# Optimization experiments

Measured on AMD Instinct MI355X. Metric: run time of the kernel, lower is better.

Reference implementation:

```python
import jax, jax.numpy as jnp
import numpy as np

H = 16
D_MODEL = 1024
D_HEAD = D_MODEL // H  # 64


def _xavier(key, shape):
    # xavier_uniform over last two dims (matches torch init on [h, in, out])
    fan_in, fan_out = shape[-2], shape[-1]
    limit = float(np.sqrt(6.0 / (fan_in + fan_out)))
    return jax.random.uniform(key, shape, jnp.float32, -limit, limit)


def setup_inputs() -> dict:
    key = jax.random.key(0)
    ks = jax.random.split(key, 7)
    B, S = 4, 2048
    x_q = jax.random.normal(ks[0], (B, S, D_MODEL), jnp.float32)
    x_k = jax.random.normal(ks[1], (B, S, D_MODEL), jnp.float32)
    x_v = jax.random.normal(ks[2], (B, S, D_MODEL), jnp.float32)
    W_Q = _xavier(ks[3], (H, D_MODEL, D_HEAD))
    W_K = _xavier(ks[4], (H, D_MODEL, D_HEAD))
    W_V = _xavier(ks[5], (H, D_MODEL, D_HEAD))
    # torch Linear weight: [out_features, in_features], y = x @ W^T
    lim = float(np.sqrt(6.0 / (2 * D_MODEL)))  # kaiming-uniform-ish default approximated by xavier for reproducibility
    W_O = jax.random.uniform(ks[6], (D_MODEL, D_MODEL), jnp.float32, -lim, lim)
    return {"x_q": x_q, "x_k": x_k, "x_v": x_v,
            "W_Q": W_Q, "W_K": W_K, "W_V": W_V, "W_O": W_O}


def reference(x_q, x_k, x_v, W_Q, W_K, W_V, W_O):
    d_scale = jnp.asarray(D_HEAD, jnp.float32) ** 0.25  # d_q == d_k == dim_q**(1/4)
    # per-head projections: [b,s,m] x [h,m,d] -> [b,h,s,d]
    Q = jnp.einsum('bsm,hmd->bhsd', x_q, W_Q)
    K = jnp.einsum('bsm,hmd->bhsd', x_k, W_K)
    V = jnp.einsum('bsm,hmd->bhsd', x_v, W_V)
    # column softmax over K^T: shape [b,h,d,s], softmax over dim=-2 (the d axis)
    Kt = jnp.swapaxes(K, -1, -2) / d_scale          # [b,h,d,s]
    Kt = jax.nn.softmax(Kt, axis=-2)
    A = jnp.einsum('bhds,bhse->bhde', Kt, V)        # KV precompute [b,h,d,d]
    Qs = jax.nn.softmax(Q / d_scale, axis=-1)       # row softmax over head dim
    Bt = jnp.einsum('bhsd,bhde->bhse', Qs, A)       # [b,h,s,d]
    b, h, s, d = Bt.shape
    # faithful to torch .view on contiguous [b,h,s,d] -> [b,s,h*d] (pure reshape, no transpose)
    Bt = Bt.reshape(b, s, h * d)
    return jnp.einsum('bsi,oi->bso', Bt, W_O)
```

## Files before the change

### kernel.cpp

```cpp
#include <hip/hip_runtime.h>
#include <cstdint>
#include <cstddef>

#define DMODEL 1024
#define HEADS  16
#define DHEAD  64
#define BATCH  4
#define SEQ    2048
#define ROWS   (BATCH * SEQ)
#define INV_DSCALE 0.3535533905932738f

typedef float  f32x4  __attribute__((ext_vector_type(4)));
typedef __bf16 bf16x8 __attribute__((ext_vector_type(8)));
typedef unsigned short u16x8 __attribute__((ext_vector_type(8)));

__device__ __forceinline__ unsigned short f2bf(float x) {
    union { float f; unsigned u; } c; c.f = x;
    unsigned u = c.u;
    return (unsigned short)((u + 0x7fffu + ((u >> 16) & 1u)) >> 16);
}
__device__ __forceinline__ float bf2f(unsigned short h) {
    union { unsigned u; float f; } c; c.u = ((unsigned)h) << 16;
    return c.f;
}

__device__ __forceinline__ void load_g2l16(const unsigned short* g, unsigned short* l) {
    __builtin_amdgcn_global_load_lds(
        (const __attribute__((address_space(1))) unsigned int*)g,
        (__attribute__((address_space(3))) unsigned int*)l,
        16 , 0 , 0 );
}

__global__ __launch_bounds__(256) void cast_bf16(const float4* __restrict__ X,
                                                 ushort4* __restrict__ Y, int n4) {
    int i = blockIdx.x * 256 + threadIdx.x;
    if (i < n4) {
        float4 v = X[i];
        ushort4 o;
        o.x = f2bf(v.x); o.y = f2bf(v.y); o.z = f2bf(v.z); o.w = f2bf(v.w);
        Y[i] = o;
    }
}

__global__ __launch_bounds__(256) void cast3(const float4* __restrict__ x0,
                                             const float4* __restrict__ x1,
                                             const float4* __restrict__ x2,
                                             ushort4* __restrict__ y0,
                                             ushort4* __restrict__ y1,
                                             ushort4* __restrict__ y2) {
    int which = blockIdx.x >> 13;
    int i = ((blockIdx.x & 8191) << 8) + threadIdx.x;
    const float4* X = which == 0 ? x0 : (which == 1 ? x1 : x2);
    ushort4*      Y = which == 0 ? y0 : (which == 1 ? y1 : y2);
    float4 v = X[i];
    ushort4 o;
    o.x = f2bf(v.x); o.y = f2bf(v.y); o.z = f2bf(v.z); o.w = f2bf(v.w);
    Y[i] = o;
}

__global__ __launch_bounds__(256) void pack3(const float* __restrict__ W0,
                                             const float* __restrict__ W1,
                                             const float* __restrict__ W2,
                                             unsigned short* __restrict__ T0,
                                             unsigned short* __restrict__ T1,
                                             unsigned short* __restrict__ T2) {
    __shared__ float tile[64][68];
    int blk = blockIdx.x;
    int w = blk >> 8, h = (blk >> 4) & 15, mb = blk & 15;
    const float* W = w == 0 ? W0 : (w == 1 ? W1 : W2);
    unsigned short* T = w == 0 ? T0 : (w == 1 ? T1 : T2);
    int t = threadIdx.x;
    #pragma unroll
    for (int i = 0; i < 4; ++i) {
        int f = t + 256 * i;
        int m = f >> 4, dg = (f & 15) * 4;
        *(float4*)&tile[m][dg] = *(const float4*)&W[((size_t)(h * 16 + mb) * 64 + m) * 64 + dg];
    }
    __syncthreads();
    #pragma unroll
    for (int i = 0; i < 2; ++i) {
        int f = t + 256 * i;
        int d = f >> 3, mg = f & 7;
        ushort4 a, b;
        a.x = f2bf(tile[mg * 8 + 0][d]); a.y = f2bf(tile[mg * 8 + 1][d]);
        a.z = f2bf(tile[mg * 8 + 2][d]); a.w = f2bf(tile[mg * 8 + 3][d]);
        b.x = f2bf(tile[mg * 8 + 4][d]); b.y = f2bf(tile[mg * 8 + 5][d]);
        b.z = f2bf(tile[mg * 8 + 6][d]); b.w = f2bf(tile[mg * 8 + 7][d]);
        unsigned short* dst = T + (size_t)(h * 64 + d) * DMODEL + mb * 64 + mg * 8;
        *(ushort4*)dst = a; *(ushort4*)(dst + 4) = b;
    }
}

template <bool SM, bool OBF16>
__global__ __launch_bounds__(256, 4) void gemm_bt(const unsigned short* __restrict__ A,
                                                  const unsigned short* __restrict__ B,
                                                  void* __restrict__ Cv,
                                                  int M, int N, int K) {
    __shared__ unsigned short ldsA[64 * 64];
    __shared__ unsigned short ldsB[128 * 64];

    const int t    = threadIdx.x;
    const int lane = t & 63;
    const int wave = t >> 6;
    const int bm0  = blockIdx.x * 64;
    const int bn0  = blockIdx.y * 128;
    const int wm   = (wave & 1) * 32;
    const int wn   = (wave >> 1) * 64;
    const int fr   = lane & 15;
    const int quad = lane >> 4;

    f32x4 acc[2][4] = {};

    const unsigned short* gA[2];
    const unsigned short* gB[4];
    #pragma unroll
    for (int i = 0; i < 2; ++i) {
        int f = t + 256 * i, row = f >> 3, kg = (f & 7) ^ (row & 7);
        gA[i] = A + (size_t)(bm0 + row) * K + kg * 8;
    }
    #pragma unroll
    for (int i = 0; i < 4; ++i) {
        int f = t + 256 * i, row = f >> 3, kg = (f & 7) ^ (row & 7);
        gB[i] = B + (size_t)(bn0 + row) * K + kg * 8;
    }

    for (int k0 = 0; k0 < K; k0 += 64) {
        #pragma unroll
        for (int i = 0; i < 2; ++i)
            load_g2l16(gA[i] + k0, &ldsA[(t + 256 * i) * 8]);
        #pragma unroll
        for (int i = 0; i < 4; ++i)
            load_g2l16(gB[i] + k0, &ldsB[(t + 256 * i) * 8]);
        asm volatile("s_waitcnt vmcnt(0)" ::: "memory");
        __syncthreads();

        bf16x8 af[2][2], bfr[4][2];
        #pragma unroll
        for (int i = 0; i < 2; ++i) {
            int row = wm + i * 16 + fr;
            #pragma unroll
            for (int kh = 0; kh < 2; ++kh) {
                int s = (kh * 4 + quad) ^ (row & 7);
                af[i][kh] = *reinterpret_cast<const bf16x8*>(&ldsA[row * 64 + s * 8]);
            }
        }
        #pragma unroll
        for (int j = 0; j < 4; ++j) {
            int row = wn + j * 16 + fr;
            #pragma unroll
            for (int kh = 0; kh < 2; ++kh) {
                int s = (kh * 4 + quad) ^ (row & 7);
                bfr[j][kh] = *reinterpret_cast<const bf16x8*>(&ldsB[row * 64 + s * 8]);
            }
        }

        #pragma unroll
        for (int kh = 0; kh < 2; ++kh)
            #pragma unroll
            for (int i = 0; i < 2; ++i)
                #pragma unroll
                for (int j = 0; j < 4; ++j)
                    acc[i][j] = __builtin_amdgcn_mfma_f32_16x16x32_bf16(af[i][kh], bfr[j][kh], acc[i][j], 0, 0, 0);

        __syncthreads();
    }

    #pragma unroll
    for (int i = 0; i < 2; ++i) {
        #pragma unroll
        for (int r = 0; r < 4; ++r) {
            float v[4];
            #pragma unroll
            for (int j = 0; j < 4; ++j) v[j] = acc[i][j][r];
            if (SM) {
                #pragma unroll
                for (int j = 0; j < 4; ++j) v[j] *= INV_DSCALE;
                float m = fmaxf(fmaxf(v[0], v[1]), fmaxf(v[2], v[3]));
                #pragma unroll
                for (int off = 8; off; off >>= 1) m = fmaxf(m, __shfl_xor(m, off, 16));
                float s = 0.f;
                #pragma unroll
                for (int j = 0; j < 4; ++j) { v[j] = __expf(v[j] - m); s += v[j]; }
                #pragma unroll
                for (int off = 8; off; off >>= 1) s += __shfl_xor(s, off, 16);
                float inv = 1.0f / s;
                #pragma unroll
                for (int j = 0; j < 4; ++j) v[j] *= inv;
            }
            int rr = bm0 + wm + i * 16 + quad * 4 + r;
            size_t base = (size_t)rr * N + bn0 + wn + fr;
            if (OBF16) {
                unsigned short* C = (unsigned short*)Cv;
                #pragma unroll
                for (int j = 0; j < 4; ++j) C[base + j * 16] = f2bf(v[j]);
            } else {
                float* C = (float*)Cv;
                #pragma unroll
                for (int j = 0; j < 4; ++j) C[base + j * 16] = v[j];
            }
        }
    }
}

__global__ __launch_bounds__(256) void kv_outer(const unsigned short* __restrict__ Ks,
                                                const unsigned short* __restrict__ V,
                                                float* __restrict__ P) {
    __shared__ float sk[64][64];
    __shared__ float sv[64][64];
    int bh = blockIdx.x >> 4, chunk = blockIdx.x & 15;
    int b = bh >> 4, h = bh & 15;
    int t = threadIdx.x;
    int d = t & 63, eg = t >> 6;
    int e0 = eg * 16;
    float acc[16];
    #pragma unroll
    for (int j = 0; j < 16; ++j) acc[j] = 0.f;

    for (int sc = 0; sc < 2; ++sc) {
        int s0 = chunk * 128 + sc * 64;
        #pragma unroll
        for (int i = 0; i < 2; ++i) {
            int f = t + 256 * i;
            int r = f >> 3, c = (f & 7) * 8;
            size_t g = (size_t)(b * SEQ + s0 + r) * DMODEL + h * DHEAD + c;
            u16x8 kk = *(const u16x8*)&Ks[g];
            u16x8 vv = *(const u16x8*)&V[g];
            #pragma unroll
            for (int j = 0; j < 8; ++j) { sk[r][c + j] = bf2f(kk[j]); sv[r][c + j] = bf2f(vv[j]); }
        }
        __syncthreads();
        #pragma unroll 8
        for (int s = 0; s < 64; ++s) {
            float kd = sk[s][d];
            float4 v0 = *(const float4*)&sv[s][e0];
            float4 v1 = *(const float4*)&sv[s][e0 + 4];
            float4 v2 = *(const float4*)&sv[s][e0 + 8];
            float4 v3 = *(const float4*)&sv[s][e0 + 12];
            acc[0]  += kd * v0.x; acc[1]  += kd * v0.y; acc[2]  += kd * v0.z; acc[3]  += kd * v0.w;
            acc[4]  += kd * v1.x; acc[5]  += kd * v1.y; acc[6]  += kd * v1.z; acc[7]  += kd * v1.w;
            acc[8]  += kd * v2.x; acc[9]  += kd * v2.y; acc[10] += kd * v2.z; acc[11] += kd * v2.w;
            acc[12] += kd * v3.x; acc[13] += kd * v3.y; acc[14] += kd * v3.z; acc[15] += kd * v3.w;
        }
        __syncthreads();
    }
    float* Pp = P + ((size_t)chunk * 64 + bh) * 4096 + d * 64 + e0;
    #pragma unroll
    for (int j = 0; j < 16; j += 4)
        *(float4*)&Pp[j] = make_float4(acc[j], acc[j + 1], acc[j + 2], acc[j + 3]);
}

__global__ __launch_bounds__(256) void reduce_A(const float* __restrict__ P,
                                                float* __restrict__ A) {
    int idx = blockIdx.x * 256 + threadIdx.x;
    float s = 0.f;
    #pragma unroll
    for (int c = 0; c < 16; ++c) s += P[(size_t)c * (64 * 4096) + idx];
    A[idx] = s;
}

__global__ __launch_bounds__(256) void qs_a(const unsigned short* __restrict__ Qs,
                                            const float* __restrict__ A,
                                            unsigned short* __restrict__ R) {
    __shared__ float sA[64][64];
    __shared__ float sQ[64][64];
    int bh = blockIdx.x >> 5, sb = blockIdx.x & 31;
    int b = bh >> 4, h = bh & 15;
    int t = threadIdx.x;
    #pragma unroll
    for (int i = 0; i < 4; ++i) {
        int f = t + 256 * i;
        int r = f >> 4, c = (f & 15) * 4;
        *(float4*)&sA[r][c] = *(const float4*)&A[(size_t)bh * 4096 + (size_t)f * 4];
    }
    #pragma unroll
    for (int i = 0; i < 2; ++i) {
        int f = t + 256 * i;
        int r = f >> 3, c = (f & 7) * 8;
        u16x8 q = *(const u16x8*)&Qs[(size_t)(b * SEQ + sb * 64 + r) * DMODEL + h * DHEAD + c];
        #pragma unroll
        for (int j = 0; j < 8; ++j) sQ[r][c + j] = bf2f(q[j]);
    }
    __syncthreads();
    int lane = t & 63, w = t >> 6;
    float acc[16];
    #pragma unroll
    for (int r = 0; r < 16; ++r) acc[r] = 0.f;
    for (int d2 = 0; d2 < 64; d2 += 4) {
        float a0 = sA[d2][lane], a1 = sA[d2 + 1][lane];
        float a2 = sA[d2 + 2][lane], a3 = sA[d2 + 3][lane];
        #pragma unroll
        for (int r = 0; r < 16; ++r) {
            float4 q4 = *(const float4*)&sQ[w * 16 + r][d2];
            acc[r] += q4.x * a0 + q4.y * a1 + q4.z * a2 + q4.w * a3;
        }
    }
    size_t base = (size_t)bh * (SEQ * DHEAD) + (size_t)(sb * 64 + w * 16) * DHEAD + lane;
    #pragma unroll
    for (int r = 0; r < 16; ++r) R[base + (size_t)r * DHEAD] = f2bf(acc[r]);
}

extern "C" void kernel_launch(void* const* d_in, const int* in_sizes, int n_in,
                              void* d_out, int out_size, void* d_ws, size_t ws_size,
                              hipStream_t stream) {
    const float* xq = (const float*)d_in[0];
    const float* xk = (const float*)d_in[1];
    const float* xv = (const float*)d_in[2];
    const float* Wq = (const float*)d_in[3];
    const float* Wk = (const float*)d_in[4];
    const float* Wv = (const float*)d_in[5];
    const float* Wo = (const float*)d_in[6];
    float* out = (float*)d_out;
    char* ws = (char*)d_ws;

    const size_t MB = 1ull << 20;
    unsigned short* wq_t = (unsigned short*)(ws + 0 * MB);
    unsigned short* wk_t = (unsigned short*)(ws + 2 * MB);
    unsigned short* wv_t = (unsigned short*)(ws + 4 * MB);
    unsigned short* wo_b = (unsigned short*)(ws + 6 * MB);
    unsigned short* xq_b = (unsigned short*)(ws + 8 * MB);
    unsigned short* xk_b = (unsigned short*)(ws + 24 * MB);
    unsigned short* xv_b = (unsigned short*)(ws + 40 * MB);
    unsigned short* Qb = (unsigned short*)(ws + 56 * MB);
    unsigned short* Kb = (unsigned short*)(ws + 72 * MB);
    unsigned short* Vb = (unsigned short*)(ws + 88 * MB);
    float* Am = (float*)(ws + 104 * MB);
    unsigned short* R = (unsigned short*)(ws + 105 * MB);
    float* P = (float*)(ws + 121 * MB);

    pack3<<<768, 256, 0, stream>>>(Wq, Wk, Wv, wq_t, wk_t, wv_t);
    cast_bf16<<<1024, 256, 0, stream>>>((const float4*)Wo, (ushort4*)wo_b, (DMODEL * DMODEL) / 4);

    cast3<<<3 * 8192, 256, 0, stream>>>((const float4*)xq, (const float4*)xk, (const float4*)xv,
                                        (ushort4*)xq_b, (ushort4*)xk_b, (ushort4*)xv_b);

    dim3 gg(ROWS / 64, DMODEL / 128);
    gemm_bt<true,  true><<<gg, 256, 0, stream>>>(xq_b, wq_t, Qb, ROWS, DMODEL, DMODEL);
    gemm_bt<true,  true><<<gg, 256, 0, stream>>>(xk_b, wk_t, Kb, ROWS, DMODEL, DMODEL);
    gemm_bt<false, true><<<gg, 256, 0, stream>>>(xv_b, wv_t, Vb, ROWS, DMODEL, DMODEL);

    kv_outer<<<BATCH * HEADS * 16, 256, 0, stream>>>(Kb, Vb, P);
    reduce_A<<<1024, 256, 0, stream>>>(P, Am);

    qs_a<<<BATCH * HEADS * 32, 256, 0, stream>>>(Qb, Am, R);

    gemm_bt<false, false><<<gg, 256, 0, stream>>>(R, wo_b, out, ROWS, DMODEL, DMODEL);
}
```

Baseline: 308.6 us.

## Fuse fp32-to-bf16 input cast into projection GEMM and batch launches

The separate cast3 pass is removed. The three projection GEMMs now read the fp32 activations directly and convert them to bf16 as they fill LDS, which avoids writing and re-reading three 32 MB bf16 copies. The three projection GEMMs are merged into one launch using a z grid dimension, and the weight pack and Wo cast are merged into a single kernel. The cost is that A-tile loads now go through registers as synchronous fp32 loads instead of async global-to-LDS loads, which doubles A-side global traffic per tile and may reduce overlap.

```diff
diff --git a/kernel.cpp b/kernel.cpp
--- a/kernel.cpp
+++ b/kernel.cpp
@@ -24,6 +24,17 @@
     return c.f;
 }
 
+__device__ __forceinline__ unsigned cvt_pk_bf16(float a, float b) {
+#if __has_builtin(__builtin_amdgcn_cvt_pk_bf16_f32)
+    typedef __bf16 bf16x2_t __attribute__((ext_vector_type(2)));
+    union { bf16x2_t v; unsigned u; } c;
+    c.v = __builtin_amdgcn_cvt_pk_bf16_f32(a, b);
+    return c.u;
+#else
+    return (unsigned)f2bf(a) | ((unsigned)f2bf(b) << 16);
+#endif
+}
+
 __device__ __forceinline__ void load_g2l16(const unsigned short* g, unsigned short* l) {
     __builtin_amdgcn_global_load_lds(
         (const __attribute__((address_space(1))) unsigned int*)g,
@@ -31,103 +42,102 @@
         16 , 0 , 0 );
 }
 
-__global__ __launch_bounds__(256) void cast_bf16(const float4* __restrict__ X,
-                                                 ushort4* __restrict__ Y, int n4) {
-    int i = blockIdx.x * 256 + threadIdx.x;
-    if (i < n4) {
-        float4 v = X[i];
+__global__ __launch_bounds__(256) void prep_w(const float* __restrict__ W0,
+                                              const float* __restrict__ W1,
+                                              const float* __restrict__ W2,
+                                              const float* __restrict__ Wo,
+                                              unsigned short* __restrict__ T0,
+                                              unsigned short* __restrict__ T1,
+                                              unsigned short* __restrict__ T2,
+                                              unsigned short* __restrict__ To) {
+    __shared__ float tile[64][68];
+    int blk = blockIdx.x;
+    int t = threadIdx.x;
+    if (blk < 768) {
+        int w = blk >> 8, h = (blk >> 4) & 15, mb = blk & 15;
+        const float* W = w == 0 ? W0 : (w == 1 ? W1 : W2);
+        unsigned short* T = w == 0 ? T0 : (w == 1 ? T1 : T2);
+        #pragma unroll
+        for (int i = 0; i < 4; ++i) {
+            int f = t + 256 * i;
+            int m = f >> 4, dg = (f & 15) * 4;
+            *(float4*)&tile[m][dg] = *(const float4*)&W[((size_t)(h * 16 + mb) * 64 + m) * 64 + dg];
+        }
+        __syncthreads();
+        #pragma unroll
+        for (int i = 0; i < 2; ++i) {
+            int f = t + 256 * i;
+            int d = f >> 3, mg = f & 7;
+            ushort4 a, b;
+            a.x = f2bf(tile[mg * 8 + 0][d]); a.y = f2bf(tile[mg * 8 + 1][d]);
+            a.z = f2bf(tile[mg * 8 + 2][d]); a.w = f2bf(tile[mg * 8 + 3][d]);
+            b.x = f2bf(tile[mg * 8 + 4][d]); b.y = f2bf(tile[mg * 8 + 5][d]);
+            b.z = f2bf(tile[mg * 8 + 6][d]); b.w = f2bf(tile[mg * 8 + 7][d]);
+            unsigned short* dst = T + (size_t)(h * 64 + d) * DMODEL + mb * 64 + mg * 8;
+            *(ushort4*)dst = a; *(ushort4*)(dst + 4) = b;
+        }
+    } else {
+        int i = (blk - 768) * 256 + t;
+        float4 v = ((const float4*)Wo)[i];
         ushort4 o;
         o.x = f2bf(v.x); o.y = f2bf(v.y); o.z = f2bf(v.z); o.w = f2bf(v.w);
-        Y[i] = o;
-    }
-}
-
-__global__ __launch_bounds__(256) void cast3(const float4* __restrict__ x0,
-                                             const float4* __restrict__ x1,
-                                             const float4* __restrict__ x2,
-                                             ushort4* __restrict__ y0,
-                                             ushort4* __restrict__ y1,
-                                             ushort4* __restrict__ y2) {
-    int which = blockIdx.x >> 13;
-    int i = ((blockIdx.x & 8191) << 8) + threadIdx.x;
-    const float4* X = which == 0 ? x0 : (which == 1 ? x1 : x2);
-    ushort4*      Y = which == 0 ? y0 : (which == 1 ? y1 : y2);
-    float4 v = X[i];
-    ushort4 o;
-    o.x = f2bf(v.x); o.y = f2bf(v.y); o.z = f2bf(v.z); o.w = f2bf(v.w);
-    Y[i] = o;
-}
-
-__global__ __launch_bounds__(256) void pack3(const float* __restrict__ W0,
-                                             const float* __restrict__ W1,
-                                             const float* __restrict__ W2,
-                                             unsigned short* __restrict__ T0,
-                                             unsigned short* __restrict__ T1,
-                                             unsigned short* __restrict__ T2) {
-    __shared__ float tile[64][68];
-    int blk = blockIdx.x;
-    int w = blk >> 8, h = (blk >> 4) & 15, mb = blk & 15;
-    const float* W = w == 0 ? W0 : (w == 1 ? W1 : W2);
-    unsigned short* T = w == 0 ? T0 : (w == 1 ? T1 : T2);
-    int t = threadIdx.x;
-    #pragma unroll
-    for (int i = 0; i < 4; ++i) {
-        int f = t + 256 * i;
-        int m = f >> 4, dg = (f & 15) * 4;
-        *(float4*)&tile[m][dg] = *(const float4*)&W[((size_t)(h * 16 + mb) * 64 + m) * 64 + dg];
-    }
-    __syncthreads();
-    #pragma unroll
-    for (int i = 0; i < 2; ++i) {
-        int f = t + 256 * i;
-        int d = f >> 3, mg = f & 7;
-        ushort4 a, b;
-        a.x = f2bf(tile[mg * 8 + 0][d]); a.y = f2bf(tile[mg * 8 + 1][d]);
-        a.z = f2bf(tile[mg * 8 + 2][d]); a.w = f2bf(tile[mg * 8 + 3][d]);
-        b.x = f2bf(tile[mg * 8 + 4][d]); b.y = f2bf(tile[mg * 8 + 5][d]);
-        b.z = f2bf(tile[mg * 8 + 6][d]); b.w = f2bf(tile[mg * 8 + 7][d]);
-        unsigned short* dst = T + (size_t)(h * 64 + d) * DMODEL + mb * 64 + mg * 8;
-        *(ushort4*)dst = a; *(ushort4*)(dst + 4) = b;
-    }
-}
-
-template <bool SM, bool OBF16>
-__global__ __launch_bounds__(256, 4) void gemm_bt(const unsigned short* __restrict__ A,
-                                                  const unsigned short* __restrict__ B,
-                                                  void* __restrict__ Cv,
-                                                  int M, int N, int K) {
+        ((ushort4*)To)[i] = o;
+    }
+}
+
+template <bool OBF16, bool AF32>
+__device__ __forceinline__ void gemm_core(const void* __restrict__ Av,
+                                          const unsigned short* __restrict__ Bp,
+                                          void* __restrict__ Cv,
+                                          int K, int N, int bm0, int bn0, bool sm) {
     __shared__ unsigned short ldsA[64 * 64];
     __shared__ unsigned short ldsB[128 * 64];
 
     const int t    = threadIdx.x;
     const int lane = t & 63;
     const int wave = t >> 6;
-    const int bm0  = blockIdx.x * 64;
-    const int bn0  = blockIdx.y * 128;
     const int wm   = (wave & 1) * 32;
     const int wn   = (wave >> 1) * 64;
     const int fr   = lane & 15;
     const int quad = lane >> 4;
 
+    const float*          A32 = (const float*)Av;
+    const unsigned short* A16 = (const unsigned short*)Av;
+
     f32x4 acc[2][4] = {};
 
-    const unsigned short* gA[2];
-    const unsigned short* gB[4];
+    size_t offA[2];
     #pragma unroll
     for (int i = 0; i < 2; ++i) {
         int f = t + 256 * i, row = f >> 3, kg = (f & 7) ^ (row & 7);
-        gA[i] = A + (size_t)(bm0 + row) * K + kg * 8;
-    }
+        offA[i] = (size_t)(bm0 + row) * K + kg * 8;
+    }
+    const unsigned short* gB[4];
     #pragma unroll
     for (int i = 0; i < 4; ++i) {
         int f = t + 256 * i, row = f >> 3, kg = (f & 7) ^ (row & 7);
-        gB[i] = B + (size_t)(bn0 + row) * K + kg * 8;
+        gB[i] = Bp + (size_t)(bn0 + row) * K + kg * 8;
     }
 
     for (int k0 = 0; k0 < K; k0 += 64) {
-        #pragma unroll
-        for (int i = 0; i < 2; ++i)
-            load_g2l16(gA[i] + k0, &ldsA[(t + 256 * i) * 8]);
+        if (AF32) {
+            #pragma unroll
+            for (int i = 0; i < 2; ++i) {
+                const float* src = A32 + offA[i] + k0;
+                float4 lo = *(const float4*)src;
+                float4 hi = *(const float4*)(src + 4);
+                uint4 pk;
+                pk.x = cvt_pk_bf16(lo.x, lo.y);
+                pk.y = cvt_pk_bf16(lo.z, lo.w);
+                pk.z = cvt_pk_bf16(hi.x, hi.y);
+                pk.w = cvt_pk_bf16(hi.z, hi.w);
+                *(uint4*)&ldsA[(t + 256 * i) * 8] = pk;
+            }
+        } else {
+            #pragma unroll
+            for (int i = 0; i < 2; ++i)
+                load_g2l16(A16 + offA[i] + k0, &ldsA[(t + 256 * i) * 8]);
+        }
         #pragma unroll
         for (int i = 0; i < 4; ++i)
             load_g2l16(gB[i] + k0, &ldsB[(t + 256 * i) * 8]);
@@ -172,7 +182,7 @@
             float v[4];
             #pragma unroll
             for (int j = 0; j < 4; ++j) v[j] = acc[i][j][r];
-            if (SM) {
+            if (sm) {
                 #pragma unroll
                 for (int j = 0; j < 4; ++j) v[j] *= INV_DSCALE;
                 float m = fmaxf(fmaxf(v[0], v[1]), fmaxf(v[2], v[3]));
@@ -200,6 +210,28 @@
             }
         }
     }
+}
+
+__global__ __launch_bounds__(256, 4) void proj3(const float* __restrict__ xq,
+                                                const float* __restrict__ xk,
+                                                const float* __restrict__ xv,
+                                                const unsigned short* __restrict__ wq,
+                                                const unsigned short* __restrict__ wk,
+                                                const unsigned short* __restrict__ wv,
+                                                unsigned short* __restrict__ Qb,
+                                                unsigned short* __restrict__ Kb,
+                                                unsigned short* __restrict__ Vb) {
+    int z = blockIdx.z;
+    const float* A = z == 0 ? xq : (z == 1 ? xk : xv);
+    const unsigned short* B = z == 0 ? wq : (z == 1 ? wk : wv);
+    unsigned short* C = z == 0 ? Qb : (z == 1 ? Kb : Vb);
+    gemm_core<true, true>(A, B, C, DMODEL, DMODEL, blockIdx.x * 64, blockIdx.y * 128, z < 2);
+}
+
+__global__ __launch_bounds__(256, 4) void gemm_out(const unsigned short* __restrict__ R,
+                                                   const unsigned short* __restrict__ Wo,
+                                                   float* __restrict__ out) {
+    gemm_core<false, false>(R, Wo, out, DMODEL, DMODEL, blockIdx.x * 64, blockIdx.y * 128, false);
 }
 
 __global__ __launch_bounds__(256) void kv_outer(const unsigned short* __restrict__ Ks,
@@ -317,31 +349,22 @@
     unsigned short* wk_t = (unsigned short*)(ws + 2 * MB);
     unsigned short* wv_t = (unsigned short*)(ws + 4 * MB);
     unsigned short* wo_b = (unsigned short*)(ws + 6 * MB);
-    unsigned short* xq_b = (unsigned short*)(ws + 8 * MB);
-    unsigned short* xk_b = (unsigned short*)(ws + 24 * MB);
-    unsigned short* xv_b = (unsigned short*)(ws + 40 * MB);
-    unsigned short* Qb = (unsigned short*)(ws + 56 * MB);
-    unsigned short* Kb = (unsigned short*)(ws + 72 * MB);
-    unsigned short* Vb = (unsigned short*)(ws + 88 * MB);
-    float* Am = (float*)(ws + 104 * MB);
-    unsigned short* R = (unsigned short*)(ws + 105 * MB);
-    float* P = (float*)(ws + 121 * MB);
-
-    pack3<<<768, 256, 0, stream>>>(Wq, Wk, Wv, wq_t, wk_t, wv_t);
-    cast_bf16<<<1024, 256, 0, stream>>>((const float4*)Wo, (ushort4*)wo_b, (DMODEL * DMODEL) / 4);
-
-    cast3<<<3 * 8192, 256, 0, stream>>>((const float4*)xq, (const float4*)xk, (const float4*)xv,
-                                        (ushort4*)xq_b, (ushort4*)xk_b, (ushort4*)xv_b);
-
-    dim3 gg(ROWS / 64, DMODEL / 128);
-    gemm_bt<true,  true><<<gg, 256, 0, stream>>>(xq_b, wq_t, Qb, ROWS, DMODEL, DMODEL);
-    gemm_bt<true,  true><<<gg, 256, 0, stream>>>(xk_b, wk_t, Kb, ROWS, DMODEL, DMODEL);
-    gemm_bt<false, true><<<gg, 256, 0, stream>>>(xv_b, wv_t, Vb, ROWS, DMODEL, DMODEL);
+    unsigned short* Qb = (unsigned short*)(ws + 8 * MB);
+    unsigned short* Kb = (unsigned short*)(ws + 24 * MB);
+    unsigned short* Vb = (unsigned short*)(ws + 40 * MB);
+    float* Am = (float*)(ws + 56 * MB);
+    unsigned short* R = (unsigned short*)(ws + 57 * MB);
+    float* P = (float*)(ws + 73 * MB);
+
+    prep_w<<<1792, 256, 0, stream>>>(Wq, Wk, Wv, Wo, wq_t, wk_t, wv_t, wo_b);
+
+    proj3<<<dim3(ROWS / 64, DMODEL / 128, 3), 256, 0, stream>>>(
+        xq, xk, xv, wq_t, wk_t, wv_t, Qb, Kb, Vb);
 
     kv_outer<<<BATCH * HEADS * 16, 256, 0, stream>>>(Kb, Vb, P);
     reduce_A<<<1024, 256, 0, stream>>>(P, Am);
 
     qs_a<<<BATCH * HEADS * 32, 256, 0, stream>>>(Qb, Am, R);
 
-    gemm_bt<false, false><<<gg, 256, 0, stream>>>(R, wo_b, out, ROWS, DMODEL, DMODEL);
-}
+    gemm_out<<<dim3(ROWS / 64, DMODEL / 128), 256, 0, stream>>>(R, wo_b, out);
+}
```

Measured after the change: 304.4 us. About the same (-1.4%).
